# Performance work log

Hardware: AMD Instinct MI355X
Metric: run time of the kernel (lower is better)

The kernel has to match this reference:

```python
import jax, jax.numpy as jnp
import numpy as np

D_MODEL = 1024
N_HEADS = 16
N_KV = 4
GROUPS = N_HEADS // N_KV  # 4
D_K = D_MODEL // N_HEADS  # 64
ROPE_BASE = 10000.0
SCALE = float(np.sqrt(D_K))


def rope_cos_sin(T):
    # standard RoPE tables: [T, D_K]
    inv_freq = 1.0 / (ROPE_BASE ** (jnp.arange(0, D_K, 2, dtype=jnp.float32) / D_K))
    t = jnp.arange(T, dtype=jnp.float32)
    freqs = jnp.outer(t, inv_freq)                      # [T, D_K/2]
    emb = jnp.concatenate([freqs, freqs], axis=-1)      # [T, D_K]
    return jnp.cos(emb), jnp.sin(emb)


def apply_rope(x, cos, sin):
    # x: [B, H, T, D_K]; cos/sin: [T, D_K]
    x1, x2 = jnp.split(x, 2, axis=-1)
    rot = jnp.concatenate([-x2, x1], axis=-1)
    return x * cos[None, None] + rot * sin[None, None]


def setup_inputs() -> dict:
    key = jax.random.key(0)
    ks = jax.random.split(key, 7)
    B, T = 2, 2048
    w = lambda k, shape: jax.random.normal(k, shape, jnp.float32) * 0.02
    return {
        "q": jax.random.normal(ks[0], (B, T, D_MODEL), jnp.float32),
        "k": jax.random.normal(ks[1], (B, T, D_MODEL), jnp.float32),
        "v": jax.random.normal(ks[2], (B, T, D_MODEL), jnp.float32),
        "W_q": w(ks[3], (D_MODEL, N_HEADS * D_K)),
        "W_k": w(ks[4], (D_MODEL, N_KV * D_K)),
        "W_v": w(ks[5], (D_MODEL, N_KV * D_K)),
        "W_o": w(ks[6], (D_MODEL, D_MODEL)),
    }


def reference(q, k, v, W_q, W_k, W_v, W_o):
    B, T_q, _ = q.shape
    T_k = k.shape[1]
    # projections -> [B, H, T, D_K] (repeat_interleave == reshape heads as (kv, group))
    Q = (q @ W_q).reshape(B, T_q, N_HEADS, D_K).transpose(0, 2, 1, 3)
    K = (k @ W_k).reshape(B, T_k, N_KV, D_K).transpose(0, 2, 1, 3)
    V = (v @ W_v).reshape(B, T_k, N_KV, D_K).transpose(0, 2, 1, 3)
    cos_q, sin_q = rope_cos_sin(T_q)
    cos_k, sin_k = rope_cos_sin(T_k)
    Q = apply_rope(Q, cos_q, sin_q)
    K = apply_rope(K, cos_k, sin_k)
    # group query heads per kv head: [B, N_KV, GROUPS, T_q, D_K] (no K/V duplication)
    Qg = Q.reshape(B, N_KV, GROUPS, T_q, D_K)
    scores = jnp.einsum('bkgqd,bkld->bkgql', Qg, K) / SCALE  # [B,N_KV,G,T_q,T_k]
    attn = jax.nn.softmax(scores, axis=-1)
    out = jnp.einsum('bkgql,bkld->bkgqd', attn, V)           # [B,N_KV,G,T_q,D_K]
    out = out.reshape(B, N_HEADS, T_q, D_K).transpose(0, 2, 1, 3).reshape(B, T_q, N_HEADS * D_K)
    return out @ W_o
```

## Files before the change

kernel.cpp:

```cpp
#include <hip/hip_runtime.h>
#include <hip/hip_bf16.h>
#include <math.h>

#define B_ 2
#define T_ 2048
#define DM_ 1024
#define NH_ 16
#define NKV_ 4
#define G_ 4
#define DK_ 64
#define SCL 0.1803368784f

typedef __attribute__((ext_vector_type(8))) short bf16x8;
typedef __attribute__((ext_vector_type(4))) float f32x4;
typedef __attribute__((ext_vector_type(16))) float f32x16;
typedef __attribute__((ext_vector_type(8))) unsigned short u16x8;
typedef __attribute__((ext_vector_type(4))) unsigned short u16x4;

static __device__ __forceinline__ ushort f2bf(float x) {
  __hip_bfloat16 h = __float2bfloat16(x);
  return *reinterpret_cast<ushort*>(&h);
}

__global__ __launch_bounds__(256) void prep_kernel(const float* __restrict__ Wq,
                                                   const float* __restrict__ Wk,
                                                   const float* __restrict__ Wv,
                                                   const float* __restrict__ Wo,
                                                   ushort* __restrict__ WtAll,
                                                   ushort* __restrict__ Wot,
                                                   float* __restrict__ cos_t,
                                                   float* __restrict__ sin_t) {
  const int tid = threadIdx.x;
  int bid = blockIdx.x;
  if (bid < 256) {
    int idx = bid * 256 + tid;
    int t = idx >> 5, i = idx & 31;
    float invf = 1.0f / powf(10000.0f, (float)i / 32.0f);
    float ang = (float)t * invf;
    cos_t[idx] = cosf(ang);
    sin_t[idx] = sinf(ang);
    return;
  }
  bid -= 256;
  const float* W; ushort* Wt; int N, bx, by;
  if (bid < 256)      { W = Wq; Wt = WtAll;                       N = 1024; bx = bid & 15;        by = bid >> 4; }
  else if (bid < 320) { W = Wk; Wt = WtAll + (size_t)1024 * 1024; N = 256;  bx = (bid - 256) & 3; by = (bid - 256) >> 2; }
  else if (bid < 384) { W = Wv; Wt = WtAll + (size_t)1280 * 1024; N = 256;  bx = (bid - 320) & 3; by = (bid - 320) >> 2; }
  else                { W = Wo; Wt = Wot;                         N = 1024; bx = (bid - 384) & 15; by = (bid - 384) >> 4; }
  const int n0 = bx * 64, k0 = by * 64;
  __shared__ float tile[64 * 65];
#pragma unroll
  for (int it = 0; it < 4; ++it) {
    int lin = tid + it * 256;
    int r = lin >> 4, c4 = lin & 15;
    float4 v = *(const float4*)(W + (size_t)(k0 + r) * N + n0 + c4 * 4);
    tile[r * 65 + c4 * 4 + 0] = v.x;
    tile[r * 65 + c4 * 4 + 1] = v.y;
    tile[r * 65 + c4 * 4 + 2] = v.z;
    tile[r * 65 + c4 * 4 + 3] = v.w;
  }
  __syncthreads();
#pragma unroll
  for (int it = 0; it < 4; ++it) {
    int lin = tid + it * 256;
    int n = lin >> 4, c4 = lin & 15;
    u16x4 o;
#pragma unroll
    for (int j = 0; j < 4; ++j) o[j] = f2bf(tile[(c4 * 4 + j) * 65 + n]);
    *(u16x4*)(Wt + (size_t)(n0 + n) * 1024 + k0 + c4 * 4) = o;
  }
}

__global__ __launch_bounds__(256, 2) void bgemm_kernel(const float* __restrict__ Aq,
                                                       const float* __restrict__ Ak,
                                                       const float* __restrict__ Av,
                                                       const ushort* __restrict__ Abf,
                                                       const ushort* __restrict__ Bt,
                                                       ushort* __restrict__ Qb,
                                                       ushort* __restrict__ Kb,
                                                       ushort* __restrict__ Vt,
                                                       float* __restrict__ Of, int mode,
                                                       const float* __restrict__ cos_t,
                                                       const float* __restrict__ sin_t) {
  const int tid = threadIdx.x;
  const int w = tid >> 6, lane = tid & 63;
  const int lr = lane & 15, lg = lane >> 4;
  const int wm = w >> 1, wn = w & 1;
  const int n0 = blockIdx.x * 128;
  const int m0 = blockIdx.y * 128;
  const bool f32A = (mode != 3);
  const float* Af = (n0 < 1024) ? Aq : (n0 < 1280 ? Ak : Av);

  __shared__ __align__(16) ushort As[128 * 64];
  __shared__ __align__(16) ushort Bs[128 * 64];

  f32x4 acc[4][4];
#pragma unroll
  for (int mt = 0; mt < 4; ++mt)
#pragma unroll
    for (int nt = 0; nt < 4; ++nt) acc[mt][nt] = (f32x4){0.f, 0.f, 0.f, 0.f};

  const int sr = tid >> 3, sch = tid & 7;

  float4 apf[4][2];
  u16x8 apb[4];
  u16x8 bpf[4];
  if (f32A) {
#pragma unroll
    for (int it = 0; it < 4; ++it) {
      int r = sr + it * 32;
      apf[it][0] = *(const float4*)(Af + (size_t)(m0 + r) * 1024 + sch * 8);
      apf[it][1] = *(const float4*)(Af + (size_t)(m0 + r) * 1024 + sch * 8 + 4);
    }
  } else {
#pragma unroll
    for (int it = 0; it < 4; ++it) {
      int r = sr + it * 32;
      apb[it] = *(const u16x8*)(Abf + (size_t)(m0 + r) * 1024 + sch * 8);
    }
  }
#pragma unroll
  for (int it = 0; it < 4; ++it) {
    int r = sr + it * 32;
    bpf[it] = *(const u16x8*)(Bt + (size_t)(n0 + r) * 1024 + sch * 8);
  }

  for (int kt = 0; kt < 16; ++kt) {
    __syncthreads();
#pragma unroll
    for (int it = 0; it < 4; ++it) {
      int r = sr + it * 32;
      int byte = (r * 128 + sch * 16) ^ ((r & 7) << 4);
      u16x8 aw;
      if (f32A) {
        aw[0] = f2bf(apf[it][0].x); aw[1] = f2bf(apf[it][0].y);
        aw[2] = f2bf(apf[it][0].z); aw[3] = f2bf(apf[it][0].w);
        aw[4] = f2bf(apf[it][1].x); aw[5] = f2bf(apf[it][1].y);
        aw[6] = f2bf(apf[it][1].z); aw[7] = f2bf(apf[it][1].w);
      } else {
        aw = apb[it];
      }
      *(u16x8*)((char*)As + byte) = aw;
      *(u16x8*)((char*)Bs + byte) = bpf[it];
    }
    __syncthreads();

    if (kt + 1 < 16) {
      if (f32A) {
#pragma unroll
        for (int it = 0; it < 4; ++it) {
          int r = sr + it * 32;
          apf[it][0] = *(const float4*)(Af + (size_t)(m0 + r) * 1024 + (kt + 1) * 64 + sch * 8);
          apf[it][1] = *(const float4*)(Af + (size_t)(m0 + r) * 1024 + (kt + 1) * 64 + sch * 8 + 4);
        }
      } else {
#pragma unroll
        for (int it = 0; it < 4; ++it) {
          int r = sr + it * 32;
          apb[it] = *(const u16x8*)(Abf + (size_t)(m0 + r) * 1024 + (kt + 1) * 64 + sch * 8);
        }
      }
#pragma unroll
      for (int it = 0; it < 4; ++it) {
        int r = sr + it * 32;
        bpf[it] = *(const u16x8*)(Bt + (size_t)(n0 + r) * 1024 + (kt + 1) * 64 + sch * 8);
      }
    }

    __builtin_amdgcn_s_setprio(1);
#pragma unroll
    for (int kc = 0; kc < 2; ++kc) {
      bf16x8 af[4], bfr[4];
#pragma unroll
      for (int mt = 0; mt < 4; ++mt) {
        int row = wm * 64 + mt * 16 + lr;
        int byte = (row * 128 + kc * 64 + lg * 16) ^ ((row & 7) << 4);
        af[mt] = *(bf16x8*)((char*)As + byte);
      }
#pragma unroll
      for (int nt = 0; nt < 4; ++nt) {
        int row = wn * 64 + nt * 16 + lr;
        int byte = (row * 128 + kc * 64 + lg * 16) ^ ((row & 7) << 4);
        bfr[nt] = *(bf16x8*)((char*)Bs + byte);
      }
#pragma unroll
      for (int mt = 0; mt < 4; ++mt)
#pragma unroll
        for (int nt = 0; nt < 4; ++nt)
          acc[mt][nt] = __builtin_amdgcn_mfma_f32_16x16x32_bf16(af[mt], bfr[nt], acc[mt][nt], 0, 0, 0);
    }
    __builtin_amdgcn_s_setprio(0);
  }

  const int colbase = n0 + wn * 64;
  if (mode == 3) {
#pragma unroll
    for (int mt = 0; mt < 4; ++mt) {
      int rbase = m0 + wm * 64 + mt * 16 + lg * 4;
#pragma unroll
      for (int r = 0; r < 4; ++r)
#pragma unroll
        for (int nt = 0; nt < 4; ++nt)
          Of[(size_t)(rbase + r) * DM_ + colbase + nt * 16 + lr] = acc[mt][nt][r];
    }
  } else if (colbase >= 1280) {
    int cb = colbase - 1280;
    int kvh = cb >> 6;
#pragma unroll
    for (int mt = 0; mt < 4; ++mt) {
      int row0 = m0 + wm * 64 + mt * 16 + lg * 4;
      int b = row0 >> 11, t0r = row0 & (T_ - 1);
#pragma unroll
      for (int nt = 0; nt < 4; ++nt) {
        int d = nt * 16 + lr;
        u16x4 o;
#pragma unroll
        for (int r = 0; r < 4; ++r) o[r] = f2bf(acc[mt][nt][r]);
        *(u16x4*)(Vt + ((size_t)(b * NKV_ + kvh) * DK_ + d) * T_ + t0r) = o;
      }
    }
  } else {
    const bool isQ = (colbase < 1024);
    const int cb = isQ ? colbase : (colbase - 1024);
    const int heads = isQ ? NH_ : NKV_;
    const float scl = isQ ? SCL : 1.0f;
    const int h = cb >> 6;
    ushort* O = isQ ? Qb : Kb;
#pragma unroll
    for (int mt = 0; mt < 4; ++mt) {
      int rbase = m0 + wm * 64 + mt * 16 + lg * 4;
#pragma unroll
      for (int r = 0; r < 4; ++r) {
        int row = rbase + r;
        int b = row >> 11, t = row & (T_ - 1);
#pragma unroll
        for (int nt = 0; nt < 2; ++nt) {
          int d = nt * 16 + lr;
          float c = cos_t[t * 32 + d], s = sin_t[t * 32 + d];
          float x1 = acc[mt][nt][r], x2 = acc[mt][nt + 2][r];
          size_t base = (((size_t)(b * heads + h)) * T_ + t) * DK_ + d;
          O[base] = f2bf((x1 * c - x2 * s) * scl);
          O[base + 32] = f2bf((x2 * c + x1 * s) * scl);
        }
      }
    }
  }
}

__global__ __launch_bounds__(128, 2) void attn_mfma_kernel(const ushort* __restrict__ Qb,
                                                           const ushort* __restrict__ Kb,
                                                           const ushort* __restrict__ Vt,
                                                           ushort* __restrict__ attn_out) {
  const int bid = blockIdx.x;
  const int gw = (bid & 7) * 128 + (bid >> 3);
  const int hb = gw >> 5;
  const int qt = gw & 31;
  const int b = hb >> 4;
  const int kv = (hb >> 2) & 3;
  const int g = hb & 3;
  const int h = kv * G_ + g;
  const int q0 = qt * 64;

  const int tid = threadIdx.x;
  const int w = tid >> 6;
  const int lane = tid & 63;
  const int l31 = lane & 31;
  const int hh = lane >> 5;

  __shared__ __align__(16) ushort Ks[2][64 * 64];
  __shared__ __align__(16) ushort Vs[2][64 * 64];

  const ushort* Qg = Qb + ((size_t)(b * NH_ + h) * T_ + q0 + w * 32) * DK_;
  const ushort* Kg = Kb + (size_t)(b * NKV_ + kv) * T_ * DK_;
  const ushort* Vg = Vt + (size_t)(b * NKV_ + kv) * DK_ * T_;

  bf16x8 aq[4];
#pragma unroll
  for (int ks = 0; ks < 4; ++ks)
    aq[ks] = *(const bf16x8*)(Qg + (size_t)l31 * DK_ + ks * 16 + hh * 8);

  f32x16 oacc0{}, oacc1{};
  float l_run = 0.f;

  const int sr = tid >> 3, sch = tid & 7;
  const int vcol0b = 8 * (sch & 1) + 32 * (sch >> 1);
  u16x8 kreg[4], vreg[4];

#define LOADT(t)                                                                    \
  {                                                                                 \
    _Pragma("unroll") for (int it = 0; it < 4; ++it) {                              \
      int r = sr + it * 16;                                                         \
      kreg[it] = *(const u16x8*)(Kg + (size_t)((t) * 64 + r) * DK_ + sch * 8);      \
      vreg[it] = *(const u16x8*)(Vg + (size_t)r * T_ + (t) * 64 + sch * 8);         \
    }                                                                               \
  }
#define STAGEW(bufi)                                                                \
  {                                                                                 \
    _Pragma("unroll") for (int it = 0; it < 4; ++it) {                              \
      int r = sr + it * 16;                                                         \
      int swz = (r & 7) << 4;                                                       \
      *(u16x8*)((char*)Ks[bufi] + ((r * 128 + sch * 16) ^ swz)) = kreg[it];         \
      int vx = (r * 128 + vcol0b) ^ swz;                                            \
      u16x4 lo, hi;                                                                 \
      _Pragma("unroll") for (int j = 0; j < 4; ++j) { lo[j] = vreg[it][j]; hi[j] = vreg[it][4 + j]; } \
      *(u16x4*)((char*)Vs[bufi] + vx) = lo;                                         \
      *(u16x4*)((char*)Vs[bufi] + (vx ^ 16)) = hi;                                  \
    }                                                                               \
  }

  LOADT(0);
  STAGEW(0);
  LOADT(1);
  __syncthreads();

  const int swf = (l31 & 7) << 4;

  for (int kt = 0; kt < T_ / 64; ++kt) {
    const int cur = kt & 1;
    if (kt + 1 < T_ / 64) STAGEW(cur ^ 1);
    if (kt + 2 < T_ / 64) LOADT(kt + 2);

    f32x16 st0{}, st1{};
    __builtin_amdgcn_s_setprio(1);
#pragma unroll
    for (int ks = 0; ks < 4; ++ks) {
      bf16x8 ak0 = *(bf16x8*)((char*)Ks[cur] + ((l31 * 128 + ks * 32 + hh * 16) ^ swf));
      bf16x8 ak1 = *(bf16x8*)((char*)Ks[cur] + (((32 + l31) * 128 + ks * 32 + hh * 16) ^ swf));
      st0 = __builtin_amdgcn_mfma_f32_32x32x16_bf16(ak0, aq[ks], st0, 0, 0, 0);
      st1 = __builtin_amdgcn_mfma_f32_32x32x16_bf16(ak1, aq[ks], st1, 0, 0, 0);
    }
    __builtin_amdgcn_s_setprio(0);

    float ps = 0.f;
#pragma unroll
    for (int r = 0; r < 16; ++r) {
      st0[r] = __builtin_amdgcn_exp2f(st0[r]);
      st1[r] = __builtin_amdgcn_exp2f(st1[r]);
      ps += st0[r] + st1[r];
    }
    l_run += ps;

    __builtin_amdgcn_s_setprio(1);
#pragma unroll
    for (int s = 0; s < 4; ++s) {
      const int base = (s & 1) * 8;
      u16x8 pw;
#pragma unroll
      for (int j = 0; j < 8; ++j)
        pw[j] = f2bf((s < 2) ? st0[base + j] : st1[base + j]);
      bf16x8 pa = *(bf16x8*)&pw;
      bf16x8 bv0 = *(bf16x8*)((char*)Vs[cur] + ((l31 * 128 + s * 32 + hh * 16) ^ swf));
      bf16x8 bv1 = *(bf16x8*)((char*)Vs[cur] + (((32 + l31) * 128 + s * 32 + hh * 16) ^ swf));
      oacc0 = __builtin_amdgcn_mfma_f32_32x32x16_bf16(pa, bv0, oacc0, 0, 0, 0);
      oacc1 = __builtin_amdgcn_mfma_f32_32x32x16_bf16(pa, bv1, oacc1, 0, 0, 0);
    }
    __builtin_amdgcn_s_setprio(0);

    __syncthreads();
  }

  float l_tot = l_run + __shfl_xor(l_run, 32, 64);
  float inv = 1.0f / l_tot;
#pragma unroll
  for (int r = 0; r < 16; ++r) {
    int qr = (r & 3) + 8 * (r >> 2) + 4 * hh;
    float ir = __shfl(inv, qr, 64);
    int t = q0 + w * 32 + qr;
    size_t base = ((size_t)b * T_ + t) * DM_ + h * DK_;
    attn_out[base + l31] = f2bf(oacc0[r] * ir);
    attn_out[base + 32 + l31] = f2bf(oacc1[r] * ir);
  }
#undef LOADT
#undef STAGEW
}

extern "C" void kernel_launch(void* const* d_in, const int* in_sizes, int n_in,
                              void* d_out, int out_size, void* d_ws, size_t ws_size,
                              hipStream_t stream) {
  const float* q  = (const float*)d_in[0];
  const float* k  = (const float*)d_in[1];
  const float* v  = (const float*)d_in[2];
  const float* Wq = (const float*)d_in[3];
  const float* Wk = (const float*)d_in[4];
  const float* Wv = (const float*)d_in[5];
  const float* Wo = (const float*)d_in[6];
  float* out = (float*)d_out;

  char* ws = (char*)d_ws;
  size_t off = 0;
  float* cos_t  = (float*)(ws + off);  off += (size_t)T_ * 32 * 4;
  float* sin_t  = (float*)(ws + off);  off += (size_t)T_ * 32 * 4;
  ushort* Ab    = (ushort*)(ws + off); off += (size_t)4096 * 1024 * 2;
  ushort* WtAll = (ushort*)(ws + off); off += (size_t)1536 * 1024 * 2;
  ushort* Wot   = (ushort*)(ws + off); off += (size_t)1024 * 1024 * 2;
  ushort* Qb    = (ushort*)(ws + off); off += (size_t)B_ * NH_ * T_ * DK_ * 2;
  ushort* Kb    = (ushort*)(ws + off); off += (size_t)B_ * NKV_ * T_ * DK_ * 2;
  ushort* Vt    = (ushort*)(ws + off); off += (size_t)B_ * NKV_ * T_ * DK_ * 2;

  prep_kernel<<<dim3(896), dim3(256), 0, stream>>>(Wq, Wk, Wv, Wo, WtAll, Wot, cos_t, sin_t);

  bgemm_kernel<<<dim3(12, 32), dim3(256), 0, stream>>>(q, k, v, nullptr, WtAll,
                                                       Qb, Kb, Vt, nullptr, 5, cos_t, sin_t);

  attn_mfma_kernel<<<dim3(1024), dim3(128), 0, stream>>>(Qb, Kb, Vt, Ab);

  bgemm_kernel<<<dim3(8, 32), dim3(256), 0, stream>>>(nullptr, nullptr, nullptr, Ab, Wot,
                                                      nullptr, nullptr, nullptr, out, 3, cos_t, sin_t);
}
```

Measured before the change: 110.6 us.

## Split attention KV sequence across two warp groups per block and merge in LDS

The attention kernel now launches 256 threads per block. Each pair of waves handles half of the key/value sequence, using its own LDS buffer in place of double buffering, and the two partial outputs and row sums are merged through shared memory at the end. This doubles the number of waves working on each query tile, aiming to expose more parallelism and latency hiding. In exchange the load-to-compute overlap becomes serial with an extra barrier per tile, and the kernel pays an LDS reduction plus higher register and occupancy pressure under launch_bounds(256,4).

```diff
diff --git a/kernel.cpp b/kernel.cpp
--- a/kernel.cpp
+++ b/kernel.cpp
@@ -247,7 +247,7 @@
   }
 }
 
-__global__ __launch_bounds__(128, 2) void attn_mfma_kernel(const ushort* __restrict__ Qb,
+__global__ __launch_bounds__(256, 4) void attn_mfma_kernel(const ushort* __restrict__ Qb,
                                                            const ushort* __restrict__ Kb,
                                                            const ushort* __restrict__ Vt,
                                                            ushort* __restrict__ attn_out) {
@@ -262,27 +262,31 @@
   const int q0 = qt * 64;
 
   const int tid = threadIdx.x;
-  const int w = tid >> 6;
+  const int w2 = tid >> 6;
+  const int ks = w2 >> 1;
+  const int w = w2 & 1;
   const int lane = tid & 63;
   const int l31 = lane & 31;
   const int hh = lane >> 5;
 
   __shared__ __align__(16) ushort Ks[2][64 * 64];
   __shared__ __align__(16) ushort Vs[2][64 * 64];
+  __shared__ float mlx[64];
 
   const ushort* Qg = Qb + ((size_t)(b * NH_ + h) * T_ + q0 + w * 32) * DK_;
-  const ushort* Kg = Kb + (size_t)(b * NKV_ + kv) * T_ * DK_;
-  const ushort* Vg = Vt + (size_t)(b * NKV_ + kv) * DK_ * T_;
+  const ushort* Kg = Kb + (size_t)(b * NKV_ + kv) * T_ * DK_ + (size_t)ks * 1024 * DK_;
+  const ushort* Vg = Vt + (size_t)(b * NKV_ + kv) * DK_ * T_ + ks * 1024;
 
   bf16x8 aq[4];
 #pragma unroll
-  for (int ks = 0; ks < 4; ++ks)
-    aq[ks] = *(const bf16x8*)(Qg + (size_t)l31 * DK_ + ks * 16 + hh * 8);
+  for (int kq = 0; kq < 4; ++kq)
+    aq[kq] = *(const bf16x8*)(Qg + (size_t)l31 * DK_ + kq * 16 + hh * 8);
 
   f32x16 oacc0{}, oacc1{};
   float l_run = 0.f;
 
-  const int sr = tid >> 3, sch = tid & 7;
+  const int stid = tid & 127;
+  const int sr = stid >> 3, sch = stid & 7;
   const int vcol0b = 8 * (sch & 1) + 32 * (sch >> 1);
   u16x8 kreg[4], vreg[4];
 
@@ -294,40 +298,36 @@
       vreg[it] = *(const u16x8*)(Vg + (size_t)r * T_ + (t) * 64 + sch * 8);         \
     }                                                                               \
   }
-#define STAGEW(bufi)                                                                \
+#define STAGEW                                                                      \
   {                                                                                 \
     _Pragma("unroll") for (int it = 0; it < 4; ++it) {                              \
       int r = sr + it * 16;                                                         \
       int swz = (r & 7) << 4;                                                       \
-      *(u16x8*)((char*)Ks[bufi] + ((r * 128 + sch * 16) ^ swz)) = kreg[it];         \
+      *(u16x8*)((char*)Ks[ks] + ((r * 128 + sch * 16) ^ swz)) = kreg[it];           \
       int vx = (r * 128 + vcol0b) ^ swz;                                            \
       u16x4 lo, hi;                                                                 \
       _Pragma("unroll") for (int j = 0; j < 4; ++j) { lo[j] = vreg[it][j]; hi[j] = vreg[it][4 + j]; } \
-      *(u16x4*)((char*)Vs[bufi] + vx) = lo;                                         \
-      *(u16x4*)((char*)Vs[bufi] + (vx ^ 16)) = hi;                                  \
+      *(u16x4*)((char*)Vs[ks] + vx) = lo;                                           \
+      *(u16x4*)((char*)Vs[ks] + (vx ^ 16)) = hi;                                    \
     }                                                                               \
   }
 
   LOADT(0);
-  STAGEW(0);
+  STAGEW;
   LOADT(1);
   __syncthreads();
 
   const int swf = (l31 & 7) << 4;
 
-  for (int kt = 0; kt < T_ / 64; ++kt) {
-    const int cur = kt & 1;
-    if (kt + 1 < T_ / 64) STAGEW(cur ^ 1);
-    if (kt + 2 < T_ / 64) LOADT(kt + 2);
-
+  for (int kt = 0; kt < 16; ++kt) {
     f32x16 st0{}, st1{};
     __builtin_amdgcn_s_setprio(1);
 #pragma unroll
-    for (int ks = 0; ks < 4; ++ks) {
-      bf16x8 ak0 = *(bf16x8*)((char*)Ks[cur] + ((l31 * 128 + ks * 32 + hh * 16) ^ swf));
-      bf16x8 ak1 = *(bf16x8*)((char*)Ks[cur] + (((32 + l31) * 128 + ks * 32 + hh * 16) ^ swf));
-      st0 = __builtin_amdgcn_mfma_f32_32x32x16_bf16(ak0, aq[ks], st0, 0, 0, 0);
-      st1 = __builtin_amdgcn_mfma_f32_32x32x16_bf16(ak1, aq[ks], st1, 0, 0, 0);
+    for (int kq = 0; kq < 4; ++kq) {
+      bf16x8 ak0 = *(bf16x8*)((char*)Ks[ks] + ((l31 * 128 + kq * 32 + hh * 16) ^ swf));
+      bf16x8 ak1 = *(bf16x8*)((char*)Ks[ks] + (((32 + l31) * 128 + kq * 32 + hh * 16) ^ swf));
+      st0 = __builtin_amdgcn_mfma_f32_32x32x16_bf16(ak0, aq[kq], st0, 0, 0, 0);
+      st1 = __builtin_amdgcn_mfma_f32_32x32x16_bf16(ak1, aq[kq], st1, 0, 0, 0);
     }
     __builtin_amdgcn_s_setprio(0);
 
@@ -349,26 +349,47 @@
       for (int j = 0; j < 8; ++j)
         pw[j] = f2bf((s < 2) ? st0[base + j] : st1[base + j]);
       bf16x8 pa = *(bf16x8*)&pw;
-      bf16x8 bv0 = *(bf16x8*)((char*)Vs[cur] + ((l31 * 128 + s * 32 + hh * 16) ^ swf));
-      bf16x8 bv1 = *(bf16x8*)((char*)Vs[cur] + (((32 + l31) * 128 + s * 32 + hh * 16) ^ swf));
+      bf16x8 bv0 = *(bf16x8*)((char*)Vs[ks] + ((l31 * 128 + s * 32 + hh * 16) ^ swf));
+      bf16x8 bv1 = *(bf16x8*)((char*)Vs[ks] + (((32 + l31) * 128 + s * 32 + hh * 16) ^ swf));
       oacc0 = __builtin_amdgcn_mfma_f32_32x32x16_bf16(pa, bv0, oacc0, 0, 0, 0);
       oacc1 = __builtin_amdgcn_mfma_f32_32x32x16_bf16(pa, bv1, oacc1, 0, 0, 0);
     }
     __builtin_amdgcn_s_setprio(0);
 
     __syncthreads();
-  }
-
-  float l_tot = l_run + __shfl_xor(l_run, 32, 64);
-  float inv = 1.0f / l_tot;
-#pragma unroll
-  for (int r = 0; r < 16; ++r) {
-    int qr = (r & 3) + 8 * (r >> 2) + 4 * hh;
-    float ir = __shfl(inv, qr, 64);
-    int t = q0 + w * 32 + qr;
-    size_t base = ((size_t)b * T_ + t) * DM_ + h * DK_;
-    attn_out[base + l31] = f2bf(oacc0[r] * ir);
-    attn_out[base + 32 + l31] = f2bf(oacc1[r] * ir);
+    if (kt + 1 < 16) {
+      STAGEW;
+      if (kt + 2 < 16) LOADT(kt + 2);
+      __syncthreads();
+    }
+  }
+
+  float l_half = l_run + __shfl_xor(l_run, 32, 64);
+
+  float* mrgO = (float*)(&Ks[0][0]);
+  if (ks == 1) {
+#pragma unroll
+    for (int r = 0; r < 16; ++r) {
+      int qr = (r & 3) + 8 * (r >> 2) + 4 * hh;
+      mrgO[(w * 32 + qr) * 64 + l31] = oacc0[r];
+      mrgO[(w * 32 + qr) * 64 + 32 + l31] = oacc1[r];
+    }
+    if (hh == 0) mlx[w * 32 + l31] = l_half;
+  }
+  __syncthreads();
+  if (ks == 0) {
+    float inv = 1.0f / (l_half + mlx[w * 32 + l31]);
+#pragma unroll
+    for (int r = 0; r < 16; ++r) {
+      int qr = (r & 3) + 8 * (r >> 2) + 4 * hh;
+      float ir = __shfl(inv, qr, 64);
+      int t = q0 + w * 32 + qr;
+      size_t base = ((size_t)b * T_ + t) * DM_ + h * DK_;
+      float o0 = oacc0[r] + mrgO[(w * 32 + qr) * 64 + l31];
+      float o1 = oacc1[r] + mrgO[(w * 32 + qr) * 64 + 32 + l31];
+      attn_out[base + l31] = f2bf(o0 * ir);
+      attn_out[base + 32 + l31] = f2bf(o1 * ir);
+    }
   }
 #undef LOADT
 #undef STAGEW
@@ -402,7 +423,7 @@
   bgemm_kernel<<<dim3(12, 32), dim3(256), 0, stream>>>(q, k, v, nullptr, WtAll,
                                                        Qb, Kb, Vt, nullptr, 5, cos_t, sin_t);
 
-  attn_mfma_kernel<<<dim3(1024), dim3(128), 0, stream>>>(Qb, Kb, Vt, Ab);
+  attn_mfma_kernel<<<dim3(1024), dim3(256), 0, stream>>>(Qb, Kb, Vt, Ab);
 
   bgemm_kernel<<<dim3(8, 32), dim3(256), 0, stream>>>(nullptr, nullptr, nullptr, Ab, Wot,
                                                       nullptr, nullptr, nullptr, out, 3, cos_t, sin_t);
```

Measured after the change: 210.1 us. 1.9x slower.
